# Kernel tuning notes

Measured on AMD Instinct MI355X. Metric: run time of the kernel, lower is better.

## Reference

```python
import jax, jax.numpy as jnp
import numpy as np
from jax import lax

C = 256
B, H, W = 8, 64, 64


def dwconv(x, w, b, pad):
    # x: [B,C,H,W], w: [C,1,kh,kw] depthwise (groups=C), b: [C]
    y = lax.conv_general_dilated(
        x, w,
        window_strides=(1, 1),
        padding=pad,
        dimension_numbers=('NCHW', 'OIHW', 'NCHW'),
        feature_group_count=x.shape[1],
    )
    return y + b[None, :, None, None]


def setup_inputs() -> dict:
    key = jax.random.key(0)
    ks = jax.random.split(key, 16)
    s = 0.05
    inp = {
        'x': jax.random.normal(ks[0], (B, C, H, W), jnp.float32),
        'w0':   jax.random.normal(ks[1], (C, 1, 5, 5), jnp.float32) * s,
        'b0':   jax.random.normal(ks[2], (C,), jnp.float32) * s,
        'w0_1': jax.random.normal(ks[3], (C, 1, 1, 7), jnp.float32) * s,
        'b0_1': jax.random.normal(ks[4], (C,), jnp.float32) * s,
        'w0_2': jax.random.normal(ks[5], (C, 1, 7, 1), jnp.float32) * s,
        'b0_2': jax.random.normal(ks[6], (C,), jnp.float32) * s,
        'w1_1': jax.random.normal(ks[7], (C, 1, 1, 11), jnp.float32) * s,
        'b1_1': jax.random.normal(ks[8], (C,), jnp.float32) * s,
        'w1_2': jax.random.normal(ks[9], (C, 1, 11, 1), jnp.float32) * s,
        'b1_2': jax.random.normal(ks[10], (C,), jnp.float32) * s,
        'w2_1': jax.random.normal(ks[11], (C, 1, 1, 21), jnp.float32) * s,
        'b2_1': jax.random.normal(ks[12], (C,), jnp.float32) * s,
        'w2_2': jax.random.normal(ks[13], (C, 1, 21, 1), jnp.float32) * s,
        'b2_2': jax.random.normal(ks[14], (C,), jnp.float32) * s,
    }
    return inp


def reference(x, w0, b0, w0_1, b0_1, w0_2, b0_2,
              w1_1, b1_1, w1_2, b1_2, w2_1, b2_1, w2_2, b2_2):
    # 5x5 depthwise, pad 2
    attn = dwconv(x, w0, b0, ((2, 2), (2, 2)))
    # stage 0: 1x7 / 7x1 strips
    a0x = dwconv(attn, w0_1, b0_1, ((0, 0), (3, 3)))
    a0y = dwconv(attn, w0_2, b0_2, ((3, 3), (0, 0)))
    attn_0 = a0x * a0y
    # stage 1: 1x11 / 11x1 strips
    a1x = dwconv(a0x, w1_1, b1_1, ((0, 0), (5, 5)))
    a1y = dwconv(a0y, w1_2, b1_2, ((5, 5), (0, 0)))
    attn_1 = a1x * a1y
    # stage 2: 1x21 / 21x1 strips
    a2x = dwconv(a1x, w2_1, b2_1, ((0, 0), (10, 10)))
    a2y = dwconv(a1y, w2_2, b2_2, ((10, 10), (0, 0)))
    attn_2 = a2x * a2y
    return (attn_0, attn_1, attn_2)
```

## Files before the change

### kernel.cpp

```cpp
#include <hip/hip_runtime.h>


#define RA_W 4624
#define RB_W 4352
#define LDS_WORDS (RA_W + RB_W)

typedef float v2f __attribute__((ext_vector_type(2)));

__device__ __forceinline__ float dppsr1(float v) {
    return __int_as_float(__builtin_amdgcn_update_dpp(
        0, __float_as_int(v), 0x111, 0xF, 0xF, false));
}
__device__ __forceinline__ float dppsr2(float v) {
    return __int_as_float(__builtin_amdgcn_update_dpp(
        0, __float_as_int(v), 0x112, 0xF, 0xF, false));
}
__device__ __forceinline__ float dppsl1(float v) {
    return __int_as_float(__builtin_amdgcn_update_dpp(
        0, __float_as_int(v), 0x101, 0xF, 0xF, false));
}
__device__ __forceinline__ float dppsl2(float v) {
    return __int_as_float(__builtin_amdgcn_update_dpp(
        0, __float_as_int(v), 0x102, 0xF, 0xF, false));
}
__device__ __forceinline__ void ld4p(const float* p, v2f* w) {
    float4 q = *(const float4*)p;
    w[0].x = q.x; w[0].y = q.y; w[1].x = q.z; w[1].y = q.w;
}
__device__ __forceinline__ void st4p(float* p, v2f a, v2f b) {
    float4 q; q.x = a.x; q.y = a.y; q.z = b.x; q.w = b.y;
    *(float4*)p = q;
}
__device__ __forceinline__ float elem(const v2f* a, int e) {
    return (e & 1) ? a[e >> 1].y : a[e >> 1].x;
}

template<int K, int TAPOFF, int NP>
__device__ __forceinline__ void conv_acc(const float* __restrict__ wrow,
                                         const v2f* wnd, v2f* A) {
    #pragma unroll
    for (int v = 0; v < K; v++) {
        const float w = wrow[v];
        const int u = v + TAPOFF;
        if ((u & 1) == 0) {
            v2f wv; wv.x = w; wv.y = w;
            #pragma unroll
            for (int k = 0; k < NP; k++) A[k] += wv * wnd[(u >> 1) + k];
        } else {
            #pragma unroll
            for (int k = 0; k < NP; k++) {
                A[k].x += w * wnd[(u >> 1) + k].y;
                A[k].y += w * wnd[(u >> 1) + k + 1].x;
            }
        }
    }
}

template<int H>
__device__ __forceinline__ void sconv_pk(const float* __restrict__ wt, float bb,
                                         const v2f* a, bool pm, bool np, v2f* acc) {
    constexpr int HE = H + 1;
    float pe[HE], ne[HE];
    pe[0] = 0.f;
    #pragma unroll
    for (int i = 1; i < HE; i++) {
        float tmp = dppsr1(elem(a, 8 - HE + i));
        pe[i] = pm ? tmp : 0.f;
    }
    #pragma unroll
    for (int i = 0; i < H; i++) {
        float tmp = dppsl1(elem(a, i));
        ne[i] = np ? tmp : 0.f;
    }
    ne[H] = 0.f;
    v2f wnd[HE + 4];
    #pragma unroll
    for (int m = 0; m < HE / 2; m++) { wnd[m].x = pe[2 * m]; wnd[m].y = pe[2 * m + 1]; }
    #pragma unroll
    for (int k = 0; k < 4; k++) wnd[HE / 2 + k] = a[k];
    #pragma unroll
    for (int m = 0; m < HE / 2; m++) {
        wnd[HE / 2 + 4 + m].x = ne[2 * m]; wnd[HE / 2 + 4 + m].y = ne[2 * m + 1];
    }
    #pragma unroll
    for (int k = 0; k < 4; k++) { acc[k].x = bb; acc[k].y = bb; }
    conv_acc<2 * H + 1, 1, 4>(wt, wnd, acc);
}

__device__ __forceinline__ void sconv21_pk(const float* __restrict__ wt, float bb,
                                           const v2f* a, bool pm, bool pm2,
                                           bool np, bool np2, v2f* acc) {
    float pe[10], ne[10];
    { float t0 = dppsr2(elem(a, 6)); pe[0] = pm2 ? t0 : 0.f; }
    { float t1 = dppsr2(elem(a, 7)); pe[1] = pm2 ? t1 : 0.f; }
    #pragma unroll
    for (int i = 0; i < 8; i++) {
        float tmp = dppsr1(elem(a, i));
        pe[2 + i] = pm ? tmp : 0.f;
    }
    #pragma unroll
    for (int i = 0; i < 8; i++) {
        float tmp = dppsl1(elem(a, i));
        ne[i] = np ? tmp : 0.f;
    }
    { float t0 = dppsl2(elem(a, 0)); ne[8] = np2 ? t0 : 0.f; }
    { float t1 = dppsl2(elem(a, 1)); ne[9] = np2 ? t1 : 0.f; }
    v2f wnd[14];
    #pragma unroll
    for (int m = 0; m < 5; m++) { wnd[m].x = pe[2 * m]; wnd[m].y = pe[2 * m + 1]; }
    #pragma unroll
    for (int k = 0; k < 4; k++) wnd[5 + k] = a[k];
    #pragma unroll
    for (int m = 0; m < 5; m++) { wnd[9 + m].x = ne[2 * m]; wnd[9 + m].y = ne[2 * m + 1]; }
    #pragma unroll
    for (int k = 0; k < 4; k++) { acc[k].x = bb; acc[k].y = bb; }
    conv_acc<21, 0, 4>(wt, wnd, acc);
}

__global__ __launch_bounds__(512, 4)
void msca_fused(const float* __restrict__ x,
                const float* __restrict__ w0,   const float* __restrict__ b0,
                const float* __restrict__ w0_1, const float* __restrict__ b0_1,
                const float* __restrict__ w0_2, const float* __restrict__ b0_2,
                const float* __restrict__ w1_1, const float* __restrict__ b1_1,
                const float* __restrict__ w1_2, const float* __restrict__ b1_2,
                const float* __restrict__ w2_1, const float* __restrict__ b2_1,
                const float* __restrict__ w2_2, const float* __restrict__ b2_2,
                float* __restrict__ out)
{
    __shared__ __align__(16) float lds[LDS_WORDS];
    float* RA = lds;
    float* RB = lds + RA_W;

    const int t     = threadIdx.x;
    const int maj   = t >> 3;
    const int lane8 = t & 7;
    const int j0    = lane8 << 3;

    const bool pm  = lane8 >= 1, np  = lane8 <= 6;
    const bool pm2 = lane8 >= 2, np2 = lane8 <= 5;

    const int scat = maj ^ (lane8 << 3);
    const int rdb  = maj * 68 + ((lane8 ^ ((maj >> 3) & 7)) << 3);

    const int plane = blockIdx.x;
    const int ch    = plane & 255;

    const float* xg = x + (size_t)plane * 4096;
    float* o0 = out + (size_t)plane * 4096;
    float* o1 = o0 + 8388608;
    float* o2 = o1 + 8388608;

    v2f xp[4];
    ld4p(&xg[maj * 64 + j0], &xp[0]);
    ld4p(&xg[maj * 64 + j0 + 4], &xp[2]);
    if (t < 136) { RA[t] = 0.f; RA[t + 4488] = 0.f; }
    if (t < 256) {
        int rr = 2 + (t >> 2), cc = t & 3;
        RA[rr * 68 + (cc < 2 ? cc : cc + 64)] = 0.f;
    }
    {
        float* row = &RA[(maj + 2) * 68];
        float2 e0; e0.x = xp[0].x; e0.y = xp[0].y; *(float2*)&row[j0 + 2] = e0;
        st4p(&row[j0 + 4], xp[1], xp[2]);
        float2 e1; e1.x = xp[3].x; e1.y = xp[3].y; *(float2*)&row[j0 + 8] = e1;
    }
    __syncthreads();

    v2f attn[4];
    {
        const float bb = b0[ch];
        #pragma unroll
        for (int k = 0; k < 4; k++) { attn[k].x = bb; attn[k].y = bb; }
        const float* w0p = w0 + ch * 25;
        #pragma unroll
        for (int dr = 0; dr < 5; dr++) {
            v2f wnd[6];
            if (dr == 2) {
                float t0 = dppsr1(elem(xp, 6)), t1 = dppsr1(elem(xp, 7));
                float n0 = dppsl1(elem(xp, 0)), n1 = dppsl1(elem(xp, 1));
                wnd[0].x = pm ? t0 : 0.f;  wnd[0].y = pm ? t1 : 0.f;
                #pragma unroll
                for (int k = 0; k < 4; k++) wnd[1 + k] = xp[k];
                wnd[5].x = np ? n0 : 0.f;  wnd[5].y = np ? n1 : 0.f;
            } else {
                const float* rowp = &RA[(maj + dr) * 68 + j0];
                ld4p(rowp,     &wnd[0]);
                ld4p(rowp + 4, &wnd[2]);
                ld4p(rowp + 8, &wnd[4]);
            }
            conv_acc<5, 0, 4>(w0p + dr * 5, wnd, attn);
        }
        #pragma unroll
        for (int e = 0; e < 8; e++) RB[(j0 + e) * 68 + scat] = elem(attn, e);
    }
    __syncthreads();

    v2f a0x[4];
    sconv_pk<3>(w0_1 + ch * 7, b0_1[ch], attn, pm, np, a0x);
    v2f stv[4];
    ld4p(&RB[rdb],     &stv[0]);
    ld4p(&RB[rdb + 4], &stv[2]);
    v2f a0y[4];
    sconv_pk<3>(w0_2 + ch * 7, b0_2[ch], stv, pm, np, a0y);
    #pragma unroll
    for (int d = 0; d < 8; d++) RA[(j0 + d) * 68 + scat] = elem(a0y, d);
    __syncthreads();

    v2f prod0[4];
    {
        v2f y0r[4];
        ld4p(&RA[rdb],     &y0r[0]);
        ld4p(&RA[rdb + 4], &y0r[2]);
        #pragma unroll
        for (int k = 0; k < 4; k++) prod0[k] = a0x[k] * y0r[k];
    }
    v2f a1x[4];
    sconv_pk<5>(w1_1 + ch * 11, b1_1[ch], a0x, pm, np, a1x);
    v2f a1y[4];
    sconv_pk<5>(w1_2 + ch * 11, b1_2[ch], a0y, pm, np, a1y);
    #pragma unroll
    for (int d = 0; d < 8; d++) RB[(j0 + d) * 68 + scat] = elem(a1y, d);
    __syncthreads();

    st4p(&o0[maj * 64 + j0],     prod0[0], prod0[1]);
    st4p(&o0[maj * 64 + j0 + 4], prod0[2], prod0[3]);
    v2f prod1[4];
    {
        v2f y1r[4];
        ld4p(&RB[rdb],     &y1r[0]);
        ld4p(&RB[rdb + 4], &y1r[2]);
        #pragma unroll
        for (int k = 0; k < 4; k++) prod1[k] = a1x[k] * y1r[k];
    }
    {
        v2f a2y[4];
        sconv21_pk(w2_2 + ch * 21, b2_2[ch], a1y, pm, pm2, np, np2, a2y);
        #pragma unroll
        for (int d = 0; d < 8; d++) RA[(j0 + d) * 68 + scat] = elem(a2y, d);
    }
    v2f a2x[4];
    sconv21_pk(w2_1 + ch * 21, b2_1[ch], a1x, pm, pm2, np, np2, a2x);
    __syncthreads();

    st4p(&o1[maj * 64 + j0],     prod1[0], prod1[1]);
    st4p(&o1[maj * 64 + j0 + 4], prod1[2], prod1[3]);
    {
        v2f y2r[4];
        ld4p(&RA[rdb],     &y2r[0]);
        ld4p(&RA[rdb + 4], &y2r[2]);
        v2f q0 = a2x[0] * y2r[0];
        v2f q1 = a2x[1] * y2r[1];
        v2f q2 = a2x[2] * y2r[2];
        v2f q3 = a2x[3] * y2r[3];
        st4p(&o2[maj * 64 + j0],     q0, q1);
        st4p(&o2[maj * 64 + j0 + 4], q2, q3);
    }
}

extern "C" void kernel_launch(void* const* d_in, const int* in_sizes, int n_in,
                              void* d_out, int out_size, void* d_ws, size_t ws_size,
                              hipStream_t stream) {
    msca_fused<<<2048, 512, 0, stream>>>(
        (const float*)d_in[0],
        (const float*)d_in[1],  (const float*)d_in[2],
        (const float*)d_in[3],  (const float*)d_in[4],
        (const float*)d_in[5],  (const float*)d_in[6],
        (const float*)d_in[7],  (const float*)d_in[8],
        (const float*)d_in[9],  (const float*)d_in[10],
        (const float*)d_in[11], (const float*)d_in[12],
        (const float*)d_in[13], (const float*)d_in[14],
        (float*)d_out);
}
```

Measured before the change: 41.45 us.

## Load 5x5 halo rows from global and run all vertical stages before one barrier

The 5x5 conv now reads its neighbouring rows straight from global memory (clamped and zero-masked, with DPP for the column halo) instead of staging a padded tile in LDS behind a barrier. The vertical chain (a0y, a1y, a2y) is computed in one phase into three separate transposed LDS buffers, so the horizontal chain and products follow after a single barrier. This cuts the barrier count from five to two. In exchange it raises LDS use to about 68 KB per block, which may lower blocks per CU, and does five times the global reads per thread, though those should mostly hit in cache.

Result: faster. 39.70 us, median of 2 (-4.2%).

```diff
diff --git a/kernel.cpp b/kernel.cpp
--- a/kernel.cpp
+++ b/kernel.cpp
@@ -1,9 +1,8 @@
 #include <hip/hip_runtime.h>
 
 
-#define RA_W 4624
-#define RB_W 4352
-#define LDS_WORDS (RA_W + RB_W)
+#define RW 4352
+#define LDS_WORDS (4 * RW)
 
 typedef float v2f __attribute__((ext_vector_type(2)));
 
@@ -22,6 +21,10 @@
 __device__ __forceinline__ float dppsl2(float v) {
     return __int_as_float(__builtin_amdgcn_update_dpp(
         0, __float_as_int(v), 0x102, 0xF, 0xF, false));
+}
+__device__ __forceinline__ void ld8(const float* p, float* d) {
+    float4 a = *(const float4*)p, b = *(const float4*)(p + 4);
+    d[0]=a.x; d[1]=a.y; d[2]=a.z; d[3]=a.w; d[4]=b.x; d[5]=b.y; d[6]=b.z; d[7]=b.w;
 }
 __device__ __forceinline__ void ld4p(const float* p, v2f* w) {
     float4 q = *(const float4*)p;
@@ -129,8 +132,10 @@
                 float* __restrict__ out)
 {
     __shared__ __align__(16) float lds[LDS_WORDS];
-    float* RA = lds;
-    float* RB = lds + RA_W;
+    float* RT = lds;
+    float* R0 = lds + RW;
+    float* R1 = lds + 2 * RW;
+    float* R2 = lds + 3 * RW;
 
     const int t     = threadIdx.x;
     const int maj   = t >> 3;
@@ -151,22 +156,6 @@
     float* o1 = o0 + 8388608;
     float* o2 = o1 + 8388608;
 
-    v2f xp[4];
-    ld4p(&xg[maj * 64 + j0], &xp[0]);
-    ld4p(&xg[maj * 64 + j0 + 4], &xp[2]);
-    if (t < 136) { RA[t] = 0.f; RA[t + 4488] = 0.f; }
-    if (t < 256) {
-        int rr = 2 + (t >> 2), cc = t & 3;
-        RA[rr * 68 + (cc < 2 ? cc : cc + 64)] = 0.f;
-    }
-    {
-        float* row = &RA[(maj + 2) * 68];
-        float2 e0; e0.x = xp[0].x; e0.y = xp[0].y; *(float2*)&row[j0 + 2] = e0;
-        st4p(&row[j0 + 4], xp[1], xp[2]);
-        float2 e1; e1.x = xp[3].x; e1.y = xp[3].y; *(float2*)&row[j0 + 8] = e1;
-    }
-    __syncthreads();
-
     v2f attn[4];
     {
         const float bb = b0[ch];
@@ -175,86 +164,82 @@
         const float* w0p = w0 + ch * 25;
         #pragma unroll
         for (int dr = 0; dr < 5; dr++) {
+            const int ri = maj + dr - 2;
+            const int rc = ri < 0 ? 0 : (ri > 63 ? 63 : ri);
+            const bool valid = (unsigned)ri <= 63u;
+            float a[8];
+            ld8(&xg[rc * 64 + j0], a);
+            #pragma unroll
+            for (int i = 0; i < 8; i++) a[i] = valid ? a[i] : 0.f;
+            float l0 = dppsr1(a[6]), l1 = dppsr1(a[7]);
+            float r0 = dppsl1(a[0]), r1 = dppsl1(a[1]);
             v2f wnd[6];
-            if (dr == 2) {
-                float t0 = dppsr1(elem(xp, 6)), t1 = dppsr1(elem(xp, 7));
-                float n0 = dppsl1(elem(xp, 0)), n1 = dppsl1(elem(xp, 1));
-                wnd[0].x = pm ? t0 : 0.f;  wnd[0].y = pm ? t1 : 0.f;
-                #pragma unroll
-                for (int k = 0; k < 4; k++) wnd[1 + k] = xp[k];
-                wnd[5].x = np ? n0 : 0.f;  wnd[5].y = np ? n1 : 0.f;
-            } else {
-                const float* rowp = &RA[(maj + dr) * 68 + j0];
-                ld4p(rowp,     &wnd[0]);
-                ld4p(rowp + 4, &wnd[2]);
-                ld4p(rowp + 8, &wnd[4]);
-            }
+            wnd[0].x = pm ? l0 : 0.f;  wnd[0].y = pm ? l1 : 0.f;
+            wnd[1].x = a[0]; wnd[1].y = a[1];
+            wnd[2].x = a[2]; wnd[2].y = a[3];
+            wnd[3].x = a[4]; wnd[3].y = a[5];
+            wnd[4].x = a[6]; wnd[4].y = a[7];
+            wnd[5].x = np ? r0 : 0.f;  wnd[5].y = np ? r1 : 0.f;
             conv_acc<5, 0, 4>(w0p + dr * 5, wnd, attn);
         }
         #pragma unroll
-        for (int e = 0; e < 8; e++) RB[(j0 + e) * 68 + scat] = elem(attn, e);
+        for (int e = 0; e < 8; e++) RT[(j0 + e) * 68 + scat] = elem(attn, e);
     }
     __syncthreads();
 
-    v2f a0x[4];
-    sconv_pk<3>(w0_1 + ch * 7, b0_1[ch], attn, pm, np, a0x);
-    v2f stv[4];
-    ld4p(&RB[rdb],     &stv[0]);
-    ld4p(&RB[rdb + 4], &stv[2]);
-    v2f a0y[4];
-    sconv_pk<3>(w0_2 + ch * 7, b0_2[ch], stv, pm, np, a0y);
-    #pragma unroll
-    for (int d = 0; d < 8; d++) RA[(j0 + d) * 68 + scat] = elem(a0y, d);
+    {
+        v2f stv[4];
+        ld4p(&RT[rdb],     &stv[0]);
+        ld4p(&RT[rdb + 4], &stv[2]);
+        v2f a0y[4];
+        sconv_pk<3>(w0_2 + ch * 7, b0_2[ch], stv, pm, np, a0y);
+        #pragma unroll
+        for (int d = 0; d < 8; d++) R0[(j0 + d) * 68 + scat] = elem(a0y, d);
+        v2f a1y[4];
+        sconv_pk<5>(w1_2 + ch * 11, b1_2[ch], a0y, pm, np, a1y);
+        #pragma unroll
+        for (int d = 0; d < 8; d++) R1[(j0 + d) * 68 + scat] = elem(a1y, d);
+        v2f a2y[4];
+        sconv21_pk(w2_2 + ch * 21, b2_2[ch], a1y, pm, pm2, np, np2, a2y);
+        #pragma unroll
+        for (int d = 0; d < 8; d++) R2[(j0 + d) * 68 + scat] = elem(a2y, d);
+    }
     __syncthreads();
 
-    v2f prod0[4];
     {
         v2f y0r[4];
-        ld4p(&RA[rdb],     &y0r[0]);
-        ld4p(&RA[rdb + 4], &y0r[2]);
-        #pragma unroll
-        for (int k = 0; k < 4; k++) prod0[k] = a0x[k] * y0r[k];
-    }
-    v2f a1x[4];
-    sconv_pk<5>(w1_1 + ch * 11, b1_1[ch], a0x, pm, np, a1x);
-    v2f a1y[4];
-    sconv_pk<5>(w1_2 + ch * 11, b1_2[ch], a0y, pm, np, a1y);
-    #pragma unroll
-    for (int d = 0; d < 8; d++) RB[(j0 + d) * 68 + scat] = elem(a1y, d);
-    __syncthreads();
-
-    st4p(&o0[maj * 64 + j0],     prod0[0], prod0[1]);
-    st4p(&o0[maj * 64 + j0 + 4], prod0[2], prod0[3]);
-    v2f prod1[4];
-    {
+        ld4p(&R0[rdb],     &y0r[0]);
+        ld4p(&R0[rdb + 4], &y0r[2]);
+        v2f a0x[4];
+        sconv_pk<3>(w0_1 + ch * 7, b0_1[ch], attn, pm, np, a0x);
+        {
+            v2f q0 = a0x[0] * y0r[0], q1 = a0x[1] * y0r[1];
+            v2f q2 = a0x[2] * y0r[2], q3 = a0x[3] * y0r[3];
+            st4p(&o0[maj * 64 + j0],     q0, q1);
+            st4p(&o0[maj * 64 + j0 + 4], q2, q3);
+        }
         v2f y1r[4];
-        ld4p(&RB[rdb],     &y1r[0]);
-        ld4p(&RB[rdb + 4], &y1r[2]);
-        #pragma unroll
-        for (int k = 0; k < 4; k++) prod1[k] = a1x[k] * y1r[k];
-    }
-    {
-        v2f a2y[4];
-        sconv21_pk(w2_2 + ch * 21, b2_2[ch], a1y, pm, pm2, np, np2, a2y);
-        #pragma unroll
-        for (int d = 0; d < 8; d++) RA[(j0 + d) * 68 + scat] = elem(a2y, d);
-    }
-    v2f a2x[4];
-    sconv21_pk(w2_1 + ch * 21, b2_1[ch], a1x, pm, pm2, np, np2, a2x);
-    __syncthreads();
-
-    st4p(&o1[maj * 64 + j0],     prod1[0], prod1[1]);
-    st4p(&o1[maj * 64 + j0 + 4], prod1[2], prod1[3]);
-    {
+        ld4p(&R1[rdb],     &y1r[0]);
+        ld4p(&R1[rdb + 4], &y1r[2]);
+        v2f a1x[4];
+        sconv_pk<5>(w1_1 + ch * 11, b1_1[ch], a0x, pm, np, a1x);
+        {
+            v2f q0 = a1x[0] * y1r[0], q1 = a1x[1] * y1r[1];
+            v2f q2 = a1x[2] * y1r[2], q3 = a1x[3] * y1r[3];
+            st4p(&o1[maj * 64 + j0],     q0, q1);
+            st4p(&o1[maj * 64 + j0 + 4], q2, q3);
+        }
         v2f y2r[4];
-        ld4p(&RA[rdb],     &y2r[0]);
-        ld4p(&RA[rdb + 4], &y2r[2]);
-        v2f q0 = a2x[0] * y2r[0];
-        v2f q1 = a2x[1] * y2r[1];
-        v2f q2 = a2x[2] * y2r[2];
-        v2f q3 = a2x[3] * y2r[3];
-        st4p(&o2[maj * 64 + j0],     q0, q1);
-        st4p(&o2[maj * 64 + j0 + 4], q2, q3);
+        ld4p(&R2[rdb],     &y2r[0]);
+        ld4p(&R2[rdb + 4], &y2r[2]);
+        v2f a2x[4];
+        sconv21_pk(w2_1 + ch * 21, b2_1[ch], a1x, pm, pm2, np, np2, a2x);
+        {
+            v2f q0 = a2x[0] * y2r[0], q1 = a2x[1] * y2r[1];
+            v2f q2 = a2x[2] * y2r[2], q3 = a2x[3] * y2r[3];
+            st4p(&o2[maj * 64 + j0],     q0, q1);
+            st4p(&o2[maj * 64 + j0 + 4], q2, q3);
+        }
     }
 }
 
```
